# Kernel optimization log

Hardware: AMD Instinct MI355X
Metric: run time of the kernel (lower is better)

The kernel has to match this reference:

```python
import jax, jax.numpy as jnp
import numpy as np

NUM_HEADS = 8
KEY_DIM = 16
D_HEAD = 64  # attn_ratio(4) * key_dim


def setup_inputs() -> dict:
    key = jax.random.key(0)
    ks = jax.random.split(key, 13)
    f = jnp.float32
    x = jax.random.normal(ks[0], (2, 256, 56, 56), dtype=f)
    wq = jax.random.normal(ks[1], (128, 256), dtype=f) * 0.05
    sq = jax.random.uniform(ks[2], (128,), dtype=f)
    bq = jax.random.normal(ks[3], (128,), dtype=f) * 0.05
    wk = jax.random.normal(ks[4], (128, 256), dtype=f) * 0.05
    sk = jax.random.uniform(ks[5], (128,), dtype=f)
    bk = jax.random.normal(ks[6], (128,), dtype=f) * 0.05
    wv = jax.random.normal(ks[7], (512, 256), dtype=f) * 0.05
    sv = jax.random.uniform(ks[8], (512,), dtype=f)
    bv = jax.random.normal(ks[9], (512,), dtype=f) * 0.05
    wp = jax.random.normal(ks[10], (256, 512), dtype=f) * 0.05
    sp = jax.random.uniform(ks[11], (256,), dtype=f)
    bp = jax.random.normal(ks[12], (256,), dtype=f) * 0.05
    return dict(x=x, wq=wq, sq=sq, bq=bq, wk=wk, sk=sk, bk=bk,
                wv=wv, sv=sv, bv=bv, wp=wp, sp=sp, bp=bp)


def _conv1x1_bn(x, w, s, b):
    # 1x1 conv (no bias) + folded BatchNorm (eval): per-channel affine
    y = jnp.einsum('oc,bchw->bohw', w, x)
    return y * s[None, :, None, None] + b[None, :, None, None]


def reference(x, wq, sq, bq, wk, sk, bk, wv, sv, bv, wp, sp, bp):
    b, c, h, w = x.shape
    n = h * w
    q = _conv1x1_bn(x, wq, sq, bq).reshape(b, NUM_HEADS, KEY_DIM, n)
    k = _conv1x1_bn(x, wk, sk, bk).reshape(b, NUM_HEADS, KEY_DIM, n)
    v = _conv1x1_bn(x, wv, sv, bv).reshape(b, NUM_HEADS, D_HEAD, n)
    # scores: q^T k, NO 1/sqrt(key_dim) scaling (faithful to source)
    attn = jax.nn.softmax(jnp.einsum('bhdn,bhdm->bhnm', q, k), axis=-1)
    # out = attn @ v^T -> (b,h,n,d), then back to (b, dh, H, W)
    o = jnp.einsum('bhnm,bhdm->bhdn', attn, v).reshape(b, NUM_HEADS * D_HEAD, h, w)
    return _conv1x1_bn(o, wp, sp, bp)
```

## Files before the change

kernel.cpp:

```cpp
#include <hip/hip_runtime.h>


typedef short  s16x8 __attribute__((ext_vector_type(8)));
typedef float  f32x4 __attribute__((ext_vector_type(4)));
typedef unsigned short u16;
typedef unsigned short u16x4 __attribute__((ext_vector_type(4)));

__device__ __forceinline__ u16 f2bf(float f) {
    unsigned u = __builtin_bit_cast(unsigned, f);
    u += 0x7FFF + ((u >> 16) & 1);
    return (u16)(u >> 16);
}
__device__ __forceinline__ u16 f2bf_h(float f) {
    unsigned u = __builtin_bit_cast(unsigned, f);
    return (u16)((u + 0x8000) >> 16);
}
__device__ __forceinline__ f32x4 mfma32(s16x8 a, s16x8 b, f32x4 c) {
    return __builtin_amdgcn_mfma_f32_16x16x32_bf16(a, b, c, 0, 0, 0);
}

__global__ __launch_bounds__(256) void xtw_kernel(
    const float* __restrict__ x, u16* __restrict__ xt,
    const float* __restrict__ wq, const float* __restrict__ sq,
    const float* __restrict__ wk, const float* __restrict__ sk,
    const float* __restrict__ wv, const float* __restrict__ sv,
    const float* __restrict__ wp, const float* __restrict__ sp,
    u16* __restrict__ wqb, u16* __restrict__ wkb,
    u16* __restrict__ wvb, u16* __restrict__ wpb)
{
    const int t = threadIdx.x;
    if (blockIdx.z == 2) {
        const int base = (blockIdx.y * 49 + blockIdx.x) * 256 + t;
        for (int idx = base; idx < 327680; idx += 50176) {
            if (idx < 32768)        wqb[idx] = f2bf(wq[idx] * sq[idx >> 8]);
            else if (idx < 65536)  { int j = idx - 32768;  wkb[j] = f2bf(wk[j] * sk[j >> 8]); }
            else if (idx < 196608) { int j = idx - 65536;  wvb[j] = f2bf(wv[j] * sv[j >> 8]); }
            else                   { int j = idx - 196608; wpb[j] = f2bf(wp[j] * sp[j >> 9]); }
        }
        return;
    }
    const int b = blockIdx.z, c0 = blockIdx.y * 64, n0 = blockIdx.x * 64;
    __shared__ float lds[64][65];
    const int nl = t & 63, cl = t >> 6;
    #pragma unroll
    for (int i = 0; i < 16; i++) {
        const int c = cl + i * 4;
        lds[c][nl] = x[(b * 256 + c0 + c) * 3136 + n0 + nl];
    }
    __syncthreads();
    #pragma unroll
    for (int i = 0; i < 16; i++) {
        const int n = cl + i * 4;
        xt[(b * 3136 + n0 + n) * 256 + c0 + nl] = f2bf(lds[nl][n]);
    }
}

__global__ __launch_bounds__(256, 4) void qkv_kernel(
    const u16* __restrict__ xt,
    const u16* __restrict__ wqb, const u16* __restrict__ wkb, const u16* __restrict__ wvb,
    const float* __restrict__ bq, const float* __restrict__ bk, const float* __restrict__ bv,
    u16* __restrict__ qws, u16* __restrict__ kws, u16* __restrict__ vpk)
{
    const int b = blockIdx.z, rt = blockIdx.y, n0 = blockIdx.x * 64;
    const int t = threadIdx.x, wave = t >> 6, lane = t & 63;
    const int l15 = lane & 15, quad = lane >> 4;
    const f32x4 z = {0.f, 0.f, 0.f, 0.f};

    if (rt < 4) {
        const u16* wb      = (rt < 2) ? wqb : wkb;
        const float* bias  = (rt < 2) ? bq : bk;
        u16* dst           = (rt < 2) ? qws : kws;
        const float qs     = (rt < 2) ? 1.44269504088896f : 1.0f;
        const int och0 = (rt & 1) * 64;
        const int m0   = n0 + wave * 16;
        const u16* xrow = &xt[(b * 3136 + m0 + l15) * 256 + quad * 8];
        s16x8 a8[8];
        #pragma unroll
        for (int kc8 = 0; kc8 < 8; kc8++) a8[kc8] = *(const s16x8*)&xrow[kc8 * 32];
        f32x4 acc[4] = {z, z, z, z};
        #pragma unroll
        for (int kc8 = 0; kc8 < 8; kc8++) {
            #pragma unroll
            for (int f = 0; f < 4; f++) {
                s16x8 bf = *(const s16x8*)&wb[(och0 + f * 16 + l15) * 256 + kc8 * 32 + quad * 8];
                acc[f] = mfma32(a8[kc8], bf, acc[f]);
            }
        }
        #pragma unroll
        for (int f = 0; f < 4; f++) {
            const int och = och0 + f * 16 + l15;
            const float bi = bias[och];
            const int h = och >> 4;
            #pragma unroll
            for (int r = 0; r < 4; r++) {
                const int tok = m0 + quad * 4 + r;
                dst[((b * 8 + h) * 3136 + tok) * 16 + l15] = f2bf((acc[f][r] + bi) * qs);
            }
        }
    } else {
        const int h    = rt - 4;
        const int och0 = h * 64 + wave * 16;
        const u16* arow = &wvb[(och0 + l15) * 256 + quad * 8];
        s16x8 a8[8];
        #pragma unroll
        for (int kc8 = 0; kc8 < 8; kc8++) a8[kc8] = *(const s16x8*)&arow[kc8 * 32];
        f32x4 acc[4] = {z, z, z, z};
        #pragma unroll
        for (int kc8 = 0; kc8 < 8; kc8++) {
            #pragma unroll
            for (int f = 0; f < 4; f++) {
                s16x8 bf = *(const s16x8*)&xt[(b * 3136 + n0 + f * 16 + l15) * 256 + kc8 * 32 + quad * 8];
                acc[f] = mfma32(a8[kc8], bf, acc[f]);
            }
        }
        u16* vdst = &vpk[(((b * 8 + h) * 49 + blockIdx.x) * 8) * 512];
        #pragma unroll
        for (int r = 0; r < 4; r++) {
            const float bi = bv[och0 + quad * 4 + r];
            const int lane_r8 = ((l15 >> 2) * 16 + quad * 4 + r) * 8;
            #pragma unroll
            for (int f = 0; f < 4; f++) {
                const int idx = ((f >> 1) * 4 + wave) * 512 + lane_r8 + (f & 1) * 4 + (l15 & 3);
                vdst[idx] = f2bf(acc[f][r] + bi);
            }
        }
    }
}

__global__ __launch_bounds__(64) void attn_kernel(
    const u16* __restrict__ qws, const u16* __restrict__ kws,
    const u16* __restrict__ vpk, u16* __restrict__ o_t)
{
    const int bh   = blockIdx.x;
    const int nb   = blockIdx.y * 32;
    const int lane = threadIdx.x;
    const int l15  = lane & 15, quad = lane >> 4;

    s16x8 aq[2];
    #pragma unroll
    for (int u = 0; u < 2; u++) {
        aq[u] = (s16x8){0, 0, 0, 0, 0, 0, 0, 0};
        if (quad < 2)
            aq[u] = *(const s16x8*)&qws[(bh * 3136 + nb + u * 16 + l15) * 16 + quad * 8];
    }
    s16x8 ones;
    #pragma unroll
    for (int i = 0; i < 8; i++) ones[i] = (short)0x3F80;

    const u16* krow = &kws[(bh * 3136 + l15) * 16 + (quad & 1) * 8];
    const u16* vb   = &vpk[bh * 49 * 4096 + lane * 8];

    f32x4 acc[2][4], acc5[2];
    #pragma unroll
    for (int u = 0; u < 2; u++) {
        #pragma unroll
        for (int dt = 0; dt < 4; dt++) acc[u][dt] = (f32x4){0.f, 0.f, 0.f, 0.f};
        acc5[u] = (f32x4){0.f, 0.f, 0.f, 0.f};
    }
    const f32x4 z = {0.f, 0.f, 0.f, 0.f};

    s16x8 kfA[4], vfA[8], kfB[4], vfB[8];

    auto loadK = [&](s16x8* kf, int c) {
        #pragma unroll
        for (int ii = 0; ii < 4; ii++)
            kf[ii] = *(const s16x8*)&krow[(c * 64 + ii * 16) * 16];
    };
    auto loadV = [&](s16x8* vf, int c) {
        #pragma unroll
        for (int i = 0; i < 8; i++)
            vf[i] = *(const s16x8*)&vb[(c * 8 + i) * 512];
    };
    auto compute = [&](const s16x8* kf, const s16x8* vf) {
        #pragma unroll
        for (int u = 0; u < 2; u++) {
            f32x4 s[4];
            #pragma unroll
            for (int ii = 0; ii < 4; ii++) s[ii] = mfma32(kf[ii], aq[u], z);
            s16x8 pf[2];
            #pragma unroll
            for (int c32 = 0; c32 < 2; c32++) {
                #pragma unroll
                for (int r = 0; r < 4; r++) {
                    pf[c32][r]     = (short)f2bf_h(__builtin_amdgcn_exp2f(s[2 * c32][r]));
                    pf[c32][4 + r] = (short)f2bf_h(__builtin_amdgcn_exp2f(s[2 * c32 + 1][r]));
                }
            }
            #pragma unroll
            for (int c32 = 0; c32 < 2; c32++) {
                #pragma unroll
                for (int dt = 0; dt < 4; dt++)
                    acc[u][dt] = mfma32(vf[c32 * 4 + dt], pf[c32], acc[u][dt]);
                acc5[u] = mfma32(ones, pf[c32], acc5[u]);
            }
        }
    };

    loadK(kfA, 0); loadV(vfA, 0);
    #pragma unroll 1
    for (int c = 0; c < 49; c += 2) {
        if (c + 1 < 49) { loadK(kfB, c + 1); loadV(vfB, c + 1); }
        compute(kfA, vfA);
        if (c + 2 < 49) { loadK(kfA, c + 2); loadV(vfA, c + 2); }
        if (c + 1 < 49) compute(kfB, vfB);
    }

    #pragma unroll
    for (int u = 0; u < 2; u++) {
        const float inv = 1.0f / acc5[u][0];
        u16* dst = &o_t[(((bh >> 3) * 3136) + nb + u * 16 + l15) * 512 + (bh & 7) * 64];
        #pragma unroll
        for (int dt = 0; dt < 4; dt++) {
            u16x4 o4;
            #pragma unroll
            for (int r = 0; r < 4; r++) o4[r] = f2bf(acc[u][dt][r] * inv);
            *(u16x4*)&dst[dt * 16 + quad * 4] = o4;
        }
    }
}

__global__ __launch_bounds__(256, 4) void proj_kernel(
    const u16* __restrict__ o_t, const u16* __restrict__ wpb,
    const float* __restrict__ bp, float* __restrict__ out)
{
    const int b = blockIdx.z, n0 = blockIdx.x * 32;
    const int och0 = blockIdx.y * 64 + (threadIdx.x >> 6) * 16;
    const int lane = threadIdx.x & 63;
    const int l15 = lane & 15, quad = lane >> 4;
    const f32x4 z = {0.f, 0.f, 0.f, 0.f};

    const u16* arow = &wpb[(och0 + l15) * 512 + quad * 8];
    s16x8 a8[16];
    #pragma unroll
    for (int kc = 0; kc < 16; kc++) a8[kc] = *(const s16x8*)&arow[kc * 32];
    f32x4 acc[2] = {z, z};
    #pragma unroll
    for (int kc = 0; kc < 16; kc++) {
        #pragma unroll
        for (int f = 0; f < 2; f++) {
            s16x8 bf = *(const s16x8*)&o_t[(b * 3136 + n0 + f * 16 + l15) * 512 + kc * 32 + quad * 8];
            acc[f] = mfma32(a8[kc], bf, acc[f]);
        }
    }
    #pragma unroll
    for (int r = 0; r < 4; r++) {
        const int och = och0 + quad * 4 + r;
        const float bi = bp[och];
        #pragma unroll
        for (int f = 0; f < 2; f++)
            out[(b * 256 + och) * 3136 + n0 + f * 16 + l15] = acc[f][r] + bi;
    }
}

extern "C" void kernel_launch(void* const* d_in, const int* in_sizes, int n_in,
                              void* d_out, int out_size, void* d_ws, size_t ws_size,
                              hipStream_t stream) {
    const float* x  = (const float*)d_in[0];
    const float* wq = (const float*)d_in[1];
    const float* sq = (const float*)d_in[2];
    const float* bq = (const float*)d_in[3];
    const float* wk = (const float*)d_in[4];
    const float* sk = (const float*)d_in[5];
    const float* bk = (const float*)d_in[6];
    const float* wv = (const float*)d_in[7];
    const float* sv = (const float*)d_in[8];
    const float* bv = (const float*)d_in[9];
    const float* wp = (const float*)d_in[10];
    const float* sp = (const float*)d_in[11];
    const float* bp = (const float*)d_in[12];
    float* out = (float*)d_out;

    u16* qws = (u16*)d_ws;
    u16* kws = qws + 802816;
    u16* vpk = kws + 802816;
    u16* R   = vpk + 3211264;
    u16* xt  = R;
    u16* ot  = R;
    u16* wqb = R + 3211264;
    u16* wkb = wqb + 32768;
    u16* wvb = wkb + 32768;
    u16* wpb = wvb + 131072;

    xtw_kernel<<<dim3(49, 4, 3), 256, 0, stream>>>(x, xt, wq, sq, wk, sk,
                                                   wv, sv, wp, sp,
                                                   wqb, wkb, wvb, wpb);
    qkv_kernel<<<dim3(49, 12, 2), 256, 0, stream>>>(xt, wqb, wkb, wvb,
                                                    bq, bk, bv, qws, kws, vpk);
    attn_kernel<<<dim3(16, 98), 64, 0, stream>>>(qws, kws, vpk, ot);
    proj_kernel<<<dim3(98, 4, 2), 256, 0, stream>>>(ot, wpb, bp, out);
}
```

Before: 182.2 us.

## Pre-pack operands in MFMA fragment layout and split attention KV across two waves

```diff
diff --git a/kernel.cpp b/kernel.cpp
--- a/kernel.cpp
+++ b/kernel.cpp
@@ -4,7 +4,6 @@
 typedef short  s16x8 __attribute__((ext_vector_type(8)));
 typedef float  f32x4 __attribute__((ext_vector_type(4)));
 typedef unsigned short u16;
-typedef unsigned short u16x4 __attribute__((ext_vector_type(4)));
 
 __device__ __forceinline__ u16 f2bf(float f) {
     unsigned u = __builtin_bit_cast(unsigned, f);
@@ -20,23 +19,32 @@
 }
 
 __global__ __launch_bounds__(256) void xtw_kernel(
-    const float* __restrict__ x, u16* __restrict__ xt,
+    const float* __restrict__ x, u16* __restrict__ xpk,
     const float* __restrict__ wq, const float* __restrict__ sq,
     const float* __restrict__ wk, const float* __restrict__ sk,
     const float* __restrict__ wv, const float* __restrict__ sv,
     const float* __restrict__ wp, const float* __restrict__ sp,
-    u16* __restrict__ wqb, u16* __restrict__ wkb,
-    u16* __restrict__ wvb, u16* __restrict__ wpb)
+    u16* __restrict__ wqpk, u16* __restrict__ wkpk,
+    u16* __restrict__ wvpk, u16* __restrict__ wppk)
 {
     const int t = threadIdx.x;
     if (blockIdx.z == 2) {
-        const int base = (blockIdx.y * 49 + blockIdx.x) * 256 + t;
-        for (int idx = base; idx < 327680; idx += 50176) {
-            if (idx < 32768)        wqb[idx] = f2bf(wq[idx] * sq[idx >> 8]);
-            else if (idx < 65536)  { int j = idx - 32768;  wkb[j] = f2bf(wk[j] * sk[j >> 8]); }
-            else if (idx < 196608) { int j = idx - 65536;  wvb[j] = f2bf(wv[j] * sv[j >> 8]); }
-            else                   { int j = idx - 196608; wpb[j] = f2bf(wp[j] * sp[j >> 9]); }
-        }
+        int ch = (blockIdx.y * 49 + blockIdx.x) * 256 + t;
+        const float *W, *S; u16* dst; int nkc;
+        if (ch < 4096)        { W = wq; S = sq; dst = wqpk; nkc = 8; }
+        else if (ch < 8192)   { W = wk; S = sk; dst = wkpk; nkc = 8;  ch -= 4096; }
+        else if (ch < 24576)  { W = wv; S = sv; dst = wvpk; nkc = 8;  ch -= 8192; }
+        else if (ch < 40960)  { W = wp; S = sp; dst = wppk; nkc = 16; ch -= 24576; }
+        else return;
+        const int lane = ch & 63, kc = (ch >> 6) % nkc, rt = (ch >> 6) / nkc;
+        const int l15 = lane & 15, q = lane >> 4;
+        const int row = rt * 16 + l15, C = nkc * 32;
+        const float sc = S[row];
+        const float* src = &W[row * C + kc * 32 + q * 8];
+        s16x8 o;
+        #pragma unroll
+        for (int j = 0; j < 8; j++) o[j] = (short)f2bf(src[j] * sc);
+        *(s16x8*)&dst[ch * 8] = o;
         return;
     }
     const int b = blockIdx.z, c0 = blockIdx.y * 64, n0 = blockIdx.x * 64;
@@ -49,15 +57,22 @@
     }
     __syncthreads();
     #pragma unroll
-    for (int i = 0; i < 16; i++) {
-        const int n = cl + i * 4;
-        xt[(b * 3136 + n0 + n) * 256 + c0 + nl] = f2bf(lds[nl][n]);
+    for (int rep = 0; rep < 2; rep++) {
+        const int idx = rep * 256 + t;
+        const int t16l = idx >> 7, kc8l = (idx >> 6) & 1, lane = idx & 63;
+        const int l15 = lane & 15, q = lane >> 4;
+        s16x8 o;
+        #pragma unroll
+        for (int j = 0; j < 8; j++)
+            o[j] = (short)f2bf(lds[kc8l * 32 + q * 8 + j][t16l * 16 + l15]);
+        const int tg = (n0 >> 4) + t16l, kg = (c0 >> 5) + kc8l;
+        *(s16x8*)&xpk[(((b * 196 + tg) * 8 + kg) * 64 + lane) * 8] = o;
     }
 }
 
 __global__ __launch_bounds__(256, 4) void qkv_kernel(
-    const u16* __restrict__ xt,
-    const u16* __restrict__ wqb, const u16* __restrict__ wkb, const u16* __restrict__ wvb,
+    const u16* __restrict__ xpk,
+    const u16* __restrict__ wqpk, const u16* __restrict__ wkpk, const u16* __restrict__ wvpk,
     const float* __restrict__ bq, const float* __restrict__ bk, const float* __restrict__ bv,
     u16* __restrict__ qws, u16* __restrict__ kws, u16* __restrict__ vpk)
 {
@@ -67,22 +82,23 @@
     const f32x4 z = {0.f, 0.f, 0.f, 0.f};
 
     if (rt < 4) {
-        const u16* wb      = (rt < 2) ? wqb : wkb;
+        const u16* wb      = (rt < 2) ? wqpk : wkpk;
         const float* bias  = (rt < 2) ? bq : bk;
         u16* dst           = (rt < 2) ? qws : kws;
         const float qs     = (rt < 2) ? 1.44269504088896f : 1.0f;
         const int och0 = (rt & 1) * 64;
         const int m0   = n0 + wave * 16;
-        const u16* xrow = &xt[(b * 3136 + m0 + l15) * 256 + quad * 8];
+        const int m_t  = blockIdx.x * 4 + wave;
         s16x8 a8[8];
         #pragma unroll
-        for (int kc8 = 0; kc8 < 8; kc8++) a8[kc8] = *(const s16x8*)&xrow[kc8 * 32];
+        for (int kc8 = 0; kc8 < 8; kc8++)
+            a8[kc8] = *(const s16x8*)&xpk[(((b * 196 + m_t) * 8 + kc8) * 64 + lane) * 8];
         f32x4 acc[4] = {z, z, z, z};
         #pragma unroll
         for (int kc8 = 0; kc8 < 8; kc8++) {
             #pragma unroll
             for (int f = 0; f < 4; f++) {
-                s16x8 bf = *(const s16x8*)&wb[(och0 + f * 16 + l15) * 256 + kc8 * 32 + quad * 8];
+                s16x8 bf = *(const s16x8*)&wb[((((rt & 1) * 4 + f) * 8 + kc8) * 64 + lane) * 8];
                 acc[f] = mfma32(a8[kc8], bf, acc[f]);
             }
         }
@@ -100,16 +116,16 @@
     } else {
         const int h    = rt - 4;
         const int och0 = h * 64 + wave * 16;
-        const u16* arow = &wvb[(och0 + l15) * 256 + quad * 8];
         s16x8 a8[8];
         #pragma unroll
-        for (int kc8 = 0; kc8 < 8; kc8++) a8[kc8] = *(const s16x8*)&arow[kc8 * 32];
+        for (int kc8 = 0; kc8 < 8; kc8++)
+            a8[kc8] = *(const s16x8*)&wvpk[(((h * 4 + wave) * 8 + kc8) * 64 + lane) * 8];
         f32x4 acc[4] = {z, z, z, z};
         #pragma unroll
         for (int kc8 = 0; kc8 < 8; kc8++) {
             #pragma unroll
             for (int f = 0; f < 4; f++) {
-                s16x8 bf = *(const s16x8*)&xt[(b * 3136 + n0 + f * 16 + l15) * 256 + kc8 * 32 + quad * 8];
+                s16x8 bf = *(const s16x8*)&xpk[(((b * 196 + blockIdx.x * 4 + f) * 8 + kc8) * 64 + lane) * 8];
                 acc[f] = mfma32(a8[kc8], bf, acc[f]);
             }
         }
@@ -127,13 +143,14 @@
     }
 }
 
-__global__ __launch_bounds__(64) void attn_kernel(
+__global__ __launch_bounds__(128) void attn_kernel(
     const u16* __restrict__ qws, const u16* __restrict__ kws,
-    const u16* __restrict__ vpk, u16* __restrict__ o_t)
+    const u16* __restrict__ vpk, u16* __restrict__ opk)
 {
     const int bh   = blockIdx.x;
     const int nb   = blockIdx.y * 32;
-    const int lane = threadIdx.x;
+    const int wave = threadIdx.x >> 6;
+    const int lane = threadIdx.x & 63;
     const int l15  = lane & 15, quad = lane >> 4;
 
     s16x8 aq[2];
@@ -160,7 +177,6 @@
     const f32x4 z = {0.f, 0.f, 0.f, 0.f};
 
     s16x8 kfA[4], vfA[8], kfB[4], vfB[8];
-
     auto loadK = [&](s16x8* kf, int c) {
         #pragma unroll
         for (int ii = 0; ii < 4; ii++)
@@ -196,31 +212,55 @@
         }
     };
 
-    loadK(kfA, 0); loadV(vfA, 0);
+    const int cs = wave ? 25 : 0;
+    const int ce = wave ? 49 : 25;
+    loadK(kfA, cs); loadV(vfA, cs);
     #pragma unroll 1
-    for (int c = 0; c < 49; c += 2) {
-        if (c + 1 < 49) { loadK(kfB, c + 1); loadV(vfB, c + 1); }
+    for (int c = cs; c < ce; c += 2) {
+        if (c + 1 < ce) { loadK(kfB, c + 1); loadV(vfB, c + 1); }
         compute(kfA, vfA);
-        if (c + 2 < 49) { loadK(kfA, c + 2); loadV(vfA, c + 2); }
-        if (c + 1 < 49) compute(kfB, vfB);
-    }
-
-    #pragma unroll
-    for (int u = 0; u < 2; u++) {
-        const float inv = 1.0f / acc5[u][0];
-        u16* dst = &o_t[(((bh >> 3) * 3136) + nb + u * 16 + l15) * 512 + (bh & 7) * 64];
+        if (c + 2 < ce) { loadK(kfA, c + 2); loadV(vfA, c + 2); }
+        if (c + 1 < ce) compute(kfB, vfB);
+    }
+
+    __shared__ float cmb[2][17][64];
+    {
+        const int u = 1 - wave;
+        #pragma unroll
+        for (int dt = 0; dt < 4; dt++)
+            #pragma unroll
+            for (int r = 0; r < 4; r++)
+                cmb[u][dt * 4 + r][lane] = acc[u][dt][r];
+        cmb[u][16][lane] = acc5[u][0];
+    }
+    __syncthreads();
+    {
+        const int u = wave;
+        #pragma unroll
+        for (int dt = 0; dt < 4; dt++)
+            #pragma unroll
+            for (int r = 0; r < 4; r++)
+                acc[u][dt][r] += cmb[u][dt * 4 + r][lane];
+        const float inv = 1.0f / (acc5[u][0] + cmb[u][16][lane]);
+
+        const int bq_ = bh >> 3, h = bh & 7;
+        const int tt = blockIdx.y * 2 + u;
+        u16* ob = &opk[((bq_ * 196 + tt) * 16) * 512];
         #pragma unroll
         for (int dt = 0; dt < 4; dt++) {
-            u16x4 o4;
-            #pragma unroll
-            for (int r = 0; r < 4; r++) o4[r] = f2bf(acc[u][dt][r] * inv);
-            *(u16x4*)&dst[dt * 16 + quad * 4] = o4;
+            const int kc = h * 2 + (dt >> 1);
+            #pragma unroll
+            for (int r = 0; r < 4; r++) {
+                const int w  = (dt & 1) * 16 + quad * 4 + r;
+                ob[kc * 512 + ((w >> 3) * 16 + l15) * 8 + (w & 7)] =
+                    f2bf(acc[u][dt][r] * inv);
+            }
         }
     }
 }
 
 __global__ __launch_bounds__(256, 4) void proj_kernel(
-    const u16* __restrict__ o_t, const u16* __restrict__ wpb,
+    const u16* __restrict__ opk, const u16* __restrict__ wppk,
     const float* __restrict__ bp, float* __restrict__ out)
 {
     const int b = blockIdx.z, n0 = blockIdx.x * 32;
@@ -229,16 +269,17 @@
     const int l15 = lane & 15, quad = lane >> 4;
     const f32x4 z = {0.f, 0.f, 0.f, 0.f};
 
-    const u16* arow = &wpb[(och0 + l15) * 512 + quad * 8];
+    const int och_t = blockIdx.y * 4 + (threadIdx.x >> 6);
     s16x8 a8[16];
     #pragma unroll
-    for (int kc = 0; kc < 16; kc++) a8[kc] = *(const s16x8*)&arow[kc * 32];
+    for (int kc = 0; kc < 16; kc++)
+        a8[kc] = *(const s16x8*)&wppk[((och_t * 16 + kc) * 64 + lane) * 8];
     f32x4 acc[2] = {z, z};
     #pragma unroll
     for (int kc = 0; kc < 16; kc++) {
         #pragma unroll
         for (int f = 0; f < 2; f++) {
-            s16x8 bf = *(const s16x8*)&o_t[(b * 3136 + n0 + f * 16 + l15) * 512 + kc * 32 + quad * 8];
+            s16x8 bf = *(const s16x8*)&opk[(((b * 196 + blockIdx.x * 2 + f) * 16 + kc) * 64 + lane) * 8];
             acc[f] = mfma32(a8[kc], bf, acc[f]);
         }
     }
@@ -270,22 +311,22 @@
     const float* bp = (const float*)d_in[12];
     float* out = (float*)d_out;
 
-    u16* qws = (u16*)d_ws;
-    u16* kws = qws + 802816;
-    u16* vpk = kws + 802816;
-    u16* R   = vpk + 3211264;
-    u16* xt  = R;
-    u16* ot  = R;
-    u16* wqb = R + 3211264;
-    u16* wkb = wqb + 32768;
-    u16* wvb = wkb + 32768;
-    u16* wpb = wvb + 131072;
-
-    xtw_kernel<<<dim3(49, 4, 3), 256, 0, stream>>>(x, xt, wq, sq, wk, sk,
+    u16* qws  = (u16*)d_ws;
+    u16* kws  = qws + 802816;
+    u16* vpk  = kws + 802816;
+    u16* R    = vpk + 3211264;
+    u16* xpk  = R;
+    u16* opk  = R;
+    u16* wqpk = R + 3211264;
+    u16* wkpk = wqpk + 32768;
+    u16* wvpk = wkpk + 32768;
+    u16* wppk = wvpk + 131072;
+
+    xtw_kernel<<<dim3(49, 4, 3), 256, 0, stream>>>(x, xpk, wq, sq, wk, sk,
                                                    wv, sv, wp, sp,
-                                                   wqb, wkb, wvb, wpb);
-    qkv_kernel<<<dim3(49, 12, 2), 256, 0, stream>>>(xt, wqb, wkb, wvb,
+                                                   wqpk, wkpk, wvpk, wppk);
+    qkv_kernel<<<dim3(49, 12, 2), 256, 0, stream>>>(xpk, wqpk, wkpk, wvpk,
                                                     bq, bk, bv, qws, kws, vpk);
-    attn_kernel<<<dim3(16, 98), 64, 0, stream>>>(qws, kws, vpk, ot);
-    proj_kernel<<<dim3(98, 4, 2), 256, 0, stream>>>(ot, wpb, bp, out);
-}
+    attn_kernel<<<dim3(16, 98), 128, 0, stream>>>(qws, kws, vpk, opk);
+    proj_kernel<<<dim3(98, 4, 2), 256, 0, stream>>>(opk, wppk, bp, out);
+}
```

Result: slower. 189.9 us (+4.2%).
